# Kernel tuning notes

Hardware: AMD Instinct MI355X
Metric: run time of the kernel (lower is better)

## Reference

```python
import math
import jax, jax.numpy as jnp
import numpy as np

EPS = 1e-5
KS = 8          # emb_ks == emb_hs
NH = 4          # attention heads
LOOKBACK = 5
NLAYERS = 4


def prelu(x, a):
    return jnp.where(x >= 0, x, a * x)


def ln_c(x, g, b):
    # LayerNormalization4D: stats over channel dim; note (std + eps) denominator
    mu = jnp.mean(x, 1, keepdims=True)
    var = jnp.mean((x - mu) ** 2, 1, keepdims=True)
    return (x - mu) / (jnp.sqrt(var + EPS) + EPS) * g[None, :, None, None] + b[None, :, None, None]


def ln_cf_head(x, g, b):
    # x: [H, B, E, T, F]; stats over (E, F); g, b: [H, E, F]
    mu = jnp.mean(x, (2, 4), keepdims=True)
    var = jnp.mean((x - mu) ** 2, (2, 4), keepdims=True)
    return (x - mu) / (jnp.sqrt(var + EPS) + EPS) * g[:, None, :, None, :] + b[:, None, :, None, :]


def ln_cf_proj(x, g, b):
    # x: [B, C, T, F]; stats over (C, F); g, b: [C, F]
    mu = jnp.mean(x, (1, 3), keepdims=True)
    var = jnp.mean((x - mu) ** 2, (1, 3), keepdims=True)
    return (x - mu) / (jnp.sqrt(var + EPS) + EPS) * g[None, :, None, :] + b[None, :, None, :]


def lstm(x, wih, whh, bih, bhh):
    # x: [N, T, I] -> hidden sequence [N, T, H]; PyTorch gate order i, f, g, o
    xp = jnp.einsum('nti,gi->ntg', x, wih) + bih + bhh
    H = whh.shape[1]
    N = x.shape[0]

    def step(carry, xt):
        h, c = carry
        gates = xt + h @ whh.T
        i, f, g, o = jnp.split(gates, 4, axis=-1)
        c = jax.nn.sigmoid(f) * c + jax.nn.sigmoid(i) * jnp.tanh(g)
        h = jax.nn.sigmoid(o) * jnp.tanh(c)
        return (h, c), h

    init = (jnp.zeros((N, H), x.dtype), jnp.zeros((N, H), x.dtype))
    _, hs = jax.lax.scan(step, init, jnp.swapaxes(xp, 0, 1))
    return jnp.swapaxes(hs, 0, 1)


def bilstm(x, wih, whh, bih, bhh):
    fwd = lstm(x, wih[0], whh[0], bih[0], bhh[0])
    bwd = lstm(x[:, ::-1], wih[1], whh[1], bih[1], bhh[1])[:, ::-1]
    return jnp.concatenate([fwd, bwd], -1)


def unfold1d(x):
    # non-overlapping unfold (ks == stride == KS): [N, C, L] -> [N, L//KS, C*KS]
    N, C, Lx = x.shape
    return x.reshape(N, C, Lx // KS, KS).transpose(0, 2, 1, 3).reshape(N, Lx // KS, C * KS)


def fold1d(h, w, b):
    # ConvTranspose1d with stride == kernel == KS; h: [N, Lp, D], w: [D, C, KS]
    y = jnp.einsum('nld,dck->nlck', h, w)
    N, Lp, C, K = y.shape
    return y.transpose(0, 2, 1, 3).reshape(N, C, Lp * K) + b[None, :, None]


def conv2d(x, w, b):
    y = jax.lax.conv_general_dilated(x, w, (1, 1), ((1, 1), (1, 1)),
                                     dimension_numbers=('NCHW', 'OIHW', 'NCHW'))
    return y + b[None, :, None, None]


def block(x, p):
    B, C, oT, oF = x.shape
    T = math.ceil((oT - KS) / KS) * KS + KS
    F = math.ceil((oF - KS) / KS) * KS + KS
    x = jnp.pad(x, ((0, 0), (0, 0), (0, T - oT), (0, F - oF)))
    input_ = x
    # intra (frequency) bidirectional LSTM
    z = ln_c(input_, p['intra_norm_g'], p['intra_norm_b'])
    z = z.transpose(0, 2, 1, 3).reshape(B * T, C, F)
    z = unfold1d(z)                                    # [B*T, F//KS, C*KS]
    h = bilstm(z, p['intra_wih'], p['intra_whh'], p['intra_bih'], p['intra_bhh'])
    z = fold1d(h, p['intra_lin_w'], p['intra_lin_b'])  # [B*T, C, F]
    intra = z.reshape(B, T, C, F).transpose(0, 2, 1, 3) + input_
    # inter (time) causal LSTM
    z = ln_c(intra, p['inter_norm_g'], p['inter_norm_b'])
    z = z.transpose(0, 3, 1, 2).reshape(B * F, C, T)
    z = unfold1d(z)                                    # [B*F, T//KS, C*KS]
    h = lstm(z, p['inter_wih'], p['inter_whh'], p['inter_bih'], p['inter_bhh'])
    z = fold1d(h, p['inter_lin_w'], p['inter_lin_b'])  # [B*F, C, T]
    inter = z.reshape(B, F, C, T).transpose(0, 2, 3, 1) + intra
    inter = inter[..., :oT, :oF]

    # per-head 1x1-conv QKV (batched over heads) + local causal attention
    def qkv(w, b, a, g, beta):
        y = jnp.einsum('bctf,hec->hbetf', inter, w) + b[:, None, :, None, None]
        y = prelu(y, a[:, None, None, None, None])
        return ln_cf_head(y, g, beta)

    Q = qkv(p['q_w'], p['q_b'], p['q_a'], p['q_g'], p['q_beta'])
    K = qkv(p['k_w'], p['k_b'], p['k_a'], p['k_g'], p['k_beta'])
    V = qkv(p['v_w'], p['v_b'], p['v_a'], p['v_g'], p['v_beta'])
    E = Q.shape[2]
    CV = V.shape[2]
    Qf = Q.transpose(0, 1, 3, 2, 4).reshape(NH, B, oT, E * oF)
    Kf = K.transpose(0, 1, 3, 2, 4).reshape(NH, B, oT, E * oF)
    Vf = V.transpose(0, 1, 3, 2, 4).reshape(NH, B, oT, CV * oF)
    attn = jnp.einsum('hbtd,hbsd->hbts', Qf, Kf) / jnp.sqrt(jnp.asarray(E * oF, Qf.dtype))
    t = jnp.arange(oT)
    d = t[:, None] - t[None, :]
    mask = (d >= 0) & (d <= LOOKBACK)      # causal with 5-frame lookback
    attn = jnp.where(mask, attn, -1e30)
    A = jax.nn.softmax(attn, axis=-1)
    O = jnp.einsum('hbts,hbsd->hbtd', A, Vf).reshape(NH, B, oT, CV, oF)
    O = O.transpose(1, 0, 3, 2, 4).reshape(B, NH * CV, oT, oF)
    y = jnp.einsum('bctf,dc->bdtf', O, p['proj_w']) + p['proj_b'][None, :, None, None]
    y = prelu(y, p['proj_a'])
    y = ln_cf_proj(y, p['proj_g'], p['proj_beta'])
    return y + inter


def _forward(x, conv_w, conv_b, gn_g, gn_b,
             intra_norm_g, intra_norm_b, intra_wih, intra_whh, intra_bih, intra_bhh,
             intra_lin_w, intra_lin_b,
             inter_norm_g, inter_norm_b, inter_wih, inter_whh, inter_bih, inter_bhh,
             inter_lin_w, inter_lin_b,
             q_w, q_b, q_a, q_g, q_beta,
             k_w, k_b, k_a, k_g, k_beta,
             v_w, v_b, v_a, v_g, v_beta,
             proj_w, proj_b, proj_a, proj_g, proj_beta,
             deconv_w, deconv_b):
    esti = conv2d(x, conv_w, conv_b)
    # GroupNorm(1, emb_dim): per-sample stats over (C, T, F), per-channel affine
    mu = jnp.mean(esti, (1, 2, 3), keepdims=True)
    var = jnp.mean((esti - mu) ** 2, (1, 2, 3), keepdims=True)
    esti = (esti - mu) / jnp.sqrt(var + EPS) * gn_g[None, :, None, None] + gn_b[None, :, None, None]
    stacked = dict(
        intra_norm_g=intra_norm_g, intra_norm_b=intra_norm_b,
        intra_wih=intra_wih, intra_whh=intra_whh, intra_bih=intra_bih, intra_bhh=intra_bhh,
        intra_lin_w=intra_lin_w, intra_lin_b=intra_lin_b,
        inter_norm_g=inter_norm_g, inter_norm_b=inter_norm_b,
        inter_wih=inter_wih, inter_whh=inter_whh, inter_bih=inter_bih, inter_bhh=inter_bhh,
        inter_lin_w=inter_lin_w, inter_lin_b=inter_lin_b,
        q_w=q_w, q_b=q_b, q_a=q_a, q_g=q_g, q_beta=q_beta,
        k_w=k_w, k_b=k_b, k_a=k_a, k_g=k_g, k_beta=k_beta,
        v_w=v_w, v_b=v_b, v_a=v_a, v_g=v_g, v_beta=v_beta,
        proj_w=proj_w, proj_b=proj_b, proj_a=proj_a, proj_g=proj_g, proj_beta=proj_beta,
    )
    for l in range(NLAYERS):
        p = {k: v[l] for k, v in stacked.items()}
        esti = block(esti, p)
    # ConvTranspose2d(k=3, s=1, p=1) == conv with spatially flipped, io-swapped kernel, pad 1
    w2 = jnp.flip(deconv_w, (2, 3)).transpose(1, 0, 2, 3)
    return conv2d(esti, w2, deconv_b)


def setup_inputs() -> dict:
    key = jax.random.key(0)
    keys = iter(jax.random.split(key, 80))

    def rn(shape, s=0.05):
        return jax.random.normal(next(keys), shape, jnp.float32) * s

    L, C, H, E, CV, FA = 4, 32, 256, 4, 8, 161
    IN = C * KS
    return dict(
        x=jax.random.normal(next(keys), (8, 2, 504, 161), jnp.float32),
        conv_w=rn((C, 2, 3, 3)), conv_b=jnp.zeros((C,), jnp.float32),
        gn_g=jnp.ones((C,), jnp.float32), gn_b=jnp.zeros((C,), jnp.float32),
        intra_norm_g=jnp.ones((L, C), jnp.float32), intra_norm_b=jnp.zeros((L, C), jnp.float32),
        intra_wih=rn((L, 2, 4 * H, IN)), intra_whh=rn((L, 2, 4 * H, H)),
        intra_bih=jnp.zeros((L, 2, 4 * H), jnp.float32), intra_bhh=jnp.zeros((L, 2, 4 * H), jnp.float32),
        intra_lin_w=rn((L, 2 * H, C, KS)), intra_lin_b=jnp.zeros((L, C), jnp.float32),
        inter_norm_g=jnp.ones((L, C), jnp.float32), inter_norm_b=jnp.zeros((L, C), jnp.float32),
        inter_wih=rn((L, 4 * H, IN)), inter_whh=rn((L, 4 * H, H)),
        inter_bih=jnp.zeros((L, 4 * H), jnp.float32), inter_bhh=jnp.zeros((L, 4 * H), jnp.float32),
        inter_lin_w=rn((L, H, C, KS)), inter_lin_b=jnp.zeros((L, C), jnp.float32),
        q_w=rn((L, NH, E, C)), q_b=jnp.zeros((L, NH, E), jnp.float32),
        q_a=jnp.full((L, NH), 0.25, jnp.float32),
        q_g=jnp.ones((L, NH, E, FA), jnp.float32), q_beta=jnp.zeros((L, NH, E, FA), jnp.float32),
        k_w=rn((L, NH, E, C)), k_b=jnp.zeros((L, NH, E), jnp.float32),
        k_a=jnp.full((L, NH), 0.25, jnp.float32),
        k_g=jnp.ones((L, NH, E, FA), jnp.float32), k_beta=jnp.zeros((L, NH, E, FA), jnp.float32),
        v_w=rn((L, NH, CV, C)), v_b=jnp.zeros((L, NH, CV), jnp.float32),
        v_a=jnp.full((L, NH), 0.25, jnp.float32),
        v_g=jnp.ones((L, NH, CV, FA), jnp.float32), v_beta=jnp.zeros((L, NH, CV, FA), jnp.float32),
        proj_w=rn((L, C, C)), proj_b=jnp.zeros((L, C), jnp.float32),
        proj_a=jnp.full((L,), 0.25, jnp.float32),
        proj_g=jnp.ones((L, C, FA), jnp.float32), proj_beta=jnp.zeros((L, C, FA), jnp.float32),
        deconv_w=rn((C, 2, 3, 3)), deconv_b=jnp.zeros((2,), jnp.float32),
    )


def reference(x, conv_w, conv_b, gn_g, gn_b,
              intra_norm_g, intra_norm_b, intra_wih, intra_whh, intra_bih, intra_bhh,
              intra_lin_w, intra_lin_b,
              inter_norm_g, inter_norm_b, inter_wih, inter_whh, inter_bih, inter_bhh,
              inter_lin_w, inter_lin_b,
              q_w, q_b, q_a, q_g, q_beta,
              k_w, k_b, k_a, k_g, k_beta,
              v_w, v_b, v_a, v_g, v_beta,
              proj_w, proj_b, proj_a, proj_g, proj_beta,
              deconv_w, deconv_b):
    return _forward(x, conv_w, conv_b, gn_g, gn_b,
                    intra_norm_g, intra_norm_b, intra_wih, intra_whh, intra_bih, intra_bhh,
                    intra_lin_w, intra_lin_b,
                    inter_norm_g, inter_norm_b, inter_wih, inter_whh, inter_bih, inter_bhh,
                    inter_lin_w, inter_lin_b,
                    q_w, q_b, q_a, q_g, q_beta,
                    k_w, k_b, k_a, k_g, k_beta,
                    v_w, v_b, v_a, v_g, v_beta,
                    proj_w, proj_b, proj_a, proj_g, proj_beta,
                    deconv_w, deconv_b)
```

## Files before the change

kernel.cpp:

```cpp
#include <hip/hip_runtime.h>
#include <hip/hip_bf16.h>
#include <math.h>

#define BB   8
#define CH   32
#define TT   504
#define FFp  168
#define OF   161
#define KSZ  8
#define HID  256
#define NG   1024
#define NHh  4
#define EE   4
#define CVv  8
#define N1   4032
#define N2   1344
#define LFi  21
#define LTi  63
#define EPSf 1e-5f

#define AS1 __attribute__((address_space(1)))
#define AS3 __attribute__((address_space(3)))

typedef __hip_bfloat16 bf16;
typedef __attribute__((ext_vector_type(8))) short s16x8;
typedef __attribute__((ext_vector_type(4))) float f32x4;

__device__ __forceinline__ float b2f(bf16 v) { return __bfloat162float(v); }
__device__ __forceinline__ bf16 f2b(float v) { return __float2bfloat16(v); }
__device__ __forceinline__ float us2f(unsigned short u) {
  return __uint_as_float(((unsigned)u) << 16);
}
__device__ __forceinline__ unsigned short f2bu(float v) {
  unsigned u = __float_as_uint(v);
  unsigned r = u + 0x7fffu + ((u >> 16) & 1u);
  return (unsigned short)(r >> 16);
}

__device__ __forceinline__ float sigm(float x) { return 1.f / (1.f + __expf(-x)); }
__device__ __forceinline__ float tanh_f(float x) {
  x = fminf(15.f, fmaxf(-15.f, x));
  float e = __expf(2.f * x);
  return (e - 1.f) / (e + 1.f);
}

__device__ __forceinline__ void block_reduce2(float& s1, float& s2, float* red) {
#pragma unroll
  for (int off = 32; off > 0; off >>= 1) {
    s1 += __shfl_down(s1, off, 64);
    s2 += __shfl_down(s2, off, 64);
  }
  int lane = threadIdx.x & 63, wv = threadIdx.x >> 6;
  __syncthreads();
  if (lane == 0) { red[wv * 2] = s1; red[wv * 2 + 1] = s2; }
  __syncthreads();
  s1 = red[0] + red[2] + red[4] + red[6];
  s2 = red[1] + red[3] + red[5] + red[7];
}

__global__ __launch_bounds__(192) void conv_in_k(const float* __restrict__ x,
                                                 const float* __restrict__ w,
                                                 const float* __restrict__ bias,
                                                 bf16* __restrict__ out) {
  __shared__ float xs[2 * 3 * (OF + 3)];
  int bt = blockIdx.x;
  int b = bt / TT, t = bt % TT;
  int tid = threadIdx.x;
  for (int i = tid; i < 2 * 3 * (OF + 3); i += 192) {
    int ci = i / (3 * (OF + 3));
    int rem = i % (3 * (OF + 3));
    int rr = rem / (OF + 3);
    int f = rem % (OF + 3);
    int ts = t + rr - 1;
    float v = 0.f;
    if (ts >= 0 && ts < TT && f < OF) v = x[((size_t)(b * 2 + ci) * TT + ts) * OF + f];
    xs[i] = v;
  }
  __syncthreads();
  int f = tid;
  if (f < OF) {
    float xv[2][3][3];
#pragma unroll
    for (int ci = 0; ci < 2; ci++)
#pragma unroll
      for (int kh = 0; kh < 3; kh++)
#pragma unroll
        for (int kw = 0; kw < 3; kw++) {
          int ff = f + kw - 1;
          xv[ci][kh][kw] = (ff < 0) ? 0.f : xs[(ci * 3 + kh) * (OF + 3) + ff];
        }
    for (int co = 0; co < CH; co++) {
      float acc = bias[co];
#pragma unroll
      for (int ci = 0; ci < 2; ci++)
#pragma unroll
        for (int kh = 0; kh < 3; kh++)
#pragma unroll
          for (int kw = 0; kw < 3; kw++)
            acc += xv[ci][kh][kw] * w[((co * 2 + ci) * 3 + kh) * 3 + kw];
      out[((size_t)(b * CH + co) * TT + t) * OF + f] = f2b(acc);
    }
  }
}

__global__ __launch_bounds__(256) void gn_reduce_k(const bf16* __restrict__ xin,
                                                   float* __restrict__ stats) {
  const int M = CH * TT * OF;
  int b = blockIdx.x >> 6;
  int part = blockIdx.x & 63;
  const bf16* p = xin + (size_t)b * M;
  float s1 = 0.f, s2 = 0.f;
  for (int i = part * 256 + threadIdx.x; i < M; i += 64 * 256) {
    float v = b2f(p[i]);
    s1 += v; s2 += v * v;
  }
  __shared__ float red[8];
  block_reduce2(s1, s2, red);
  if (threadIdx.x == 0) {
    atomicAdd(&stats[b * 2], s1);
    atomicAdd(&stats[b * 2 + 1], s2);
  }
}

__global__ __launch_bounds__(256) void gn_apply_k(const bf16* __restrict__ xin,
                                                  const float* __restrict__ stats,
                                                  const float* __restrict__ g,
                                                  const float* __restrict__ bb,
                                                  bf16* __restrict__ act) {
  int gid = blockIdx.x * 256 + threadIdx.x;
  int f = gid % FFp;
  int t = (gid / FFp) % TT;
  int c = (gid / (FFp * TT)) % CH;
  int b = gid / (FFp * TT * CH);
  float v = 0.f;
  if (f < OF) {
    const float M = (float)(CH * TT * OF);
    float mu = stats[b * 2] / M;
    float var = stats[b * 2 + 1] / M - mu * mu;
    float xv = b2f(xin[((size_t)(b * CH + c) * TT + t) * OF + f]);
    v = (xv - mu) * rsqrtf(var + EPSf) * g[c] + bb[c];
  }
  act[gid] = f2b(v);
}

__global__ __launch_bounds__(256) void ln_unfold_k(const bf16* __restrict__ xin,
                                                   const float* __restrict__ g,
                                                   const float* __restrict__ bb,
                                                   bf16* __restrict__ out, int mode) {
  __shared__ float sm[CH * FFp];
  __shared__ float mu_s[FFp], rs_s[FFp];
  int bt = blockIdx.x;
  int b = bt / TT, t = bt % TT;
  const bf16* base = xin + ((size_t)b * CH * TT + t) * FFp;
  for (int idx = threadIdx.x; idx < CH * FFp; idx += 256) {
    int c = idx / FFp, f = idx % FFp;
    sm[idx] = b2f(base[(size_t)c * TT * FFp + f]);
  }
  __syncthreads();
  if (threadIdx.x < FFp) {
    int f = threadIdx.x;
    float s1 = 0.f, s2 = 0.f;
#pragma unroll
    for (int c = 0; c < CH; c++) { float v = sm[c * FFp + f]; s1 += v; s2 += v * v; }
    float mu = s1 / CH;
    float var = s2 / CH - mu * mu;
    mu_s[f] = mu;
    rs_s[f] = 1.f / (sqrtf(var + EPSf) + EPSf);
  }
  __syncthreads();
  for (int idx = threadIdx.x; idx < CH * FFp; idx += 256) {
    int c = idx / FFp, f = idx % FFp;
    float v = (sm[idx] - mu_s[f]) * rs_s[f] * g[c] + bb[c];
    size_t o;
    if (mode == 0) {
      o = ((size_t)(f >> 3) * N1 + bt) * 256 + c * 8 + (f & 7);
    } else {
      int n = b * FFp + f;
      o = ((size_t)(t >> 3) * N2 + n) * 256 + c * 8 + (t & 7);
    }
    out[o] = f2b(v);
  }
}

__global__ __launch_bounds__(256) void lstm_prep_k(const float* __restrict__ wih0,
                                                   const float* __restrict__ whh0,
                                                   bf16* __restrict__ blob0) {
  int dir = blockIdx.y;
  const float* wih = wih0 + (size_t)dir * 262144;
  const float* whh = whh0 + (size_t)dir * 262144;
  unsigned short* blob = (unsigned short*)(blob0 + (size_t)dir * 524288);
  int gid = blockIdx.x * 256 + threadIdx.x;
  int lane = gid & 63;
  int ks = (gid >> 6) & 15;
  int nt = gid >> 10;
  int n = nt * 16 + (lane & 15);
  int kb = ks * 32 + (lane >> 4) * 8;
  unsigned short o8[8];
#pragma unroll
  for (int j = 0; j < 8; j++) {
    int k = kb + j;
    float v = (k < 256) ? wih[n * 256 + k] : whh[n * 256 + (k - 256)];
    o8[j] = f2bu(v);
  }
  *(uint4*)(blob + (size_t)gid * 8) = *(uint4*)o8;
}

__global__ __launch_bounds__(512) void lstm_mfma_k(const bf16* __restrict__ xz,
                                                   const bf16* __restrict__ blob0,
                                                   const float* __restrict__ bih0,
                                                   const float* __restrict__ bhh0,
                                                   bf16* __restrict__ hout,
                                                   int N, int Ls, int hstride, int bidir) {
  __shared__ __attribute__((aligned(16))) short afr[16 * 64 * 8];
  extern __shared__ __attribute__((aligned(16))) short bstage[];
  int tid = threadIdx.x;
  int w = tid >> 6, lane = tid & 63;
  int l15 = lane & 15, lq = lane >> 4;
  int dir = blockIdx.y;
  const short* blob = (const short*)(blob0 + (size_t)dir * 524288);
  const float* bih = bih0 + dir * NG;
  const float* bhh = bhh0 + dir * NG;
  int hoff = dir * 256;
  int n0 = blockIdx.x * 16;
  unsigned short* houtu = (unsigned short*)hout;
  const short* xzs = (const short*)xz;
  short* bst_w = bstage + w * 4096;

  float bias[4][2];
#pragma unroll
  for (int q = 0; q < 4; q++)
#pragma unroll
    for (int j = 0; j < 2; j++) {
      int n = q * 256 + (2 * w + j) * 16 + l15;
      bias[q][j] = bih[n] + bhh[n];
    }
  for (int i = tid; i < 8 * 64 * 8; i += 512) afr[8 * 64 * 8 + i] = 0;
  float cst[8];
#pragma unroll
  for (int i = 0; i < 8; i++) cst[i] = 0.f;

#define BQ_ISSUE(C)                                                              \
  {                                                                              \
    int a_ = (C) >> 3, r_ = (C) & 7;                                             \
    int nt_ = (r_ >> 1) * 16 + 2 * w + (r_ & 1);                                 \
    const short* gb_ = blob + (size_t)nt_ * 8192 + a_ * 2048 + lane * 8;         \
    short* lb_ = bst_w + ((C) & 1) * 2048;                                       \
    _Pragma("unroll")                                                            \
    for (int k_ = 0; k_ < 4; k_++)                                               \
      __builtin_amdgcn_global_load_lds((const AS1 void*)(gb_ + k_ * 512),        \
                                       (AS3 void*)(lb_ + k_ * 512), 16, 0, 0);   \
  }

  for (int st = 0; st < Ls; st++) {
    int t = (bidir && dir) ? (Ls - 1 - st) : st;
    {
      const short* gx = xzs + ((size_t)t * N + n0 + (lane & 15)) * 256 + (w * 4 + (lane >> 4)) * 8;
      __builtin_amdgcn_global_load_lds((const AS1 void*)gx, (AS3 void*)(afr + w * 512), 16, 0, 0);
    }
    BQ_ISSUE(0);
    BQ_ISSUE(1);
    __syncthreads();

    f32x4 acc[4][2];
#pragma unroll
    for (int q = 0; q < 4; q++)
#pragma unroll
      for (int j = 0; j < 2; j++)
        acc[q][j] = (f32x4){bias[q][j], bias[q][j], bias[q][j], bias[q][j]};

    s16x8 af[4];
#pragma unroll
    for (int c = 0; c < 32; c++) {
      int a = c >> 3, r = c & 7;
      int q = r >> 1, j = r & 1;
      if (r == 0) {
#pragma unroll
        for (int k = 0; k < 4; k++)
          af[k] = *(const s16x8*)(&afr[((a * 4 + k) * 64 + lane) * 8]);
      }
      __builtin_amdgcn_s_waitcnt(0x0F74);
      const short* lb = bst_w + (c & 1) * 2048;
#pragma unroll
      for (int k = 0; k < 4; k++) {
        s16x8 bf = *(const s16x8*)(lb + k * 512 + lane * 8);
        acc[q][j] = __builtin_amdgcn_mfma_f32_16x16x32_bf16(af[k], bf, acc[q][j], 0, 0, 0);
      }
      if (c < 30) BQ_ISSUE(c + 2);
    }
    __syncthreads();

#pragma unroll
    for (int j = 0; j < 2; j++) {
      int d = (2 * w + j) * 16 + l15;
      int slot = (8 + (d >> 5)) * 64 + ((d >> 3) & 3) * 16;
#pragma unroll
      for (int r = 0; r < 4; r++) {
        int m = lq * 4 + r;
        float iv = sigm(acc[0][j][r]);
        float fv = sigm(acc[1][j][r]);
        float gv = tanh_f(acc[2][j][r]);
        float ov = sigm(acc[3][j][r]);
        float c = fv * cst[j * 4 + r] + iv * gv;
        cst[j * 4 + r] = c;
        float h = ov * tanh_f(c);
        unsigned short hb = f2bu(h);
        houtu[((size_t)t * N + n0 + m) * hstride + hoff + d] = hb;
        afr[(slot + m) * 8 + (d & 7)] = (short)hb;
      }
    }
  }
#undef BQ_ISSUE
}

__global__ __launch_bounds__(256) void fold_gemm_k(const bf16* __restrict__ A,
                                                   const float* __restrict__ Bw,
                                                   const float* __restrict__ linb,
                                                   const bf16* __restrict__ resid,
                                                   bf16* __restrict__ outp,
                                                   int K, int mode) {
  __shared__ float As[16 * 68];
  __shared__ float Bs[16 * 64];
  int tid = threadIdx.x;
  int n0 = blockIdx.x * 64;
  int m0 = blockIdx.y * 64;
  int tr = tid >> 4, tc = tid & 15;
  float acc[4][4] = {};
  int arow = tid >> 2, akg = (tid & 3) * 4;
  int bkk = tid >> 4, bc4 = (tid & 15) * 4;
  for (int k0 = 0; k0 < K; k0 += 16) {
    ushort4 avu = *(const ushort4*)((const unsigned short*)A + (size_t)(m0 + arow) * K + k0 + akg);
    float4 bv = *(const float4*)(Bw + (size_t)(k0 + bkk) * 256 + n0 + bc4);
    __syncthreads();
    As[(akg + 0) * 68 + arow] = us2f(avu.x);
    As[(akg + 1) * 68 + arow] = us2f(avu.y);
    As[(akg + 2) * 68 + arow] = us2f(avu.z);
    As[(akg + 3) * 68 + arow] = us2f(avu.w);
    *(float4*)(&Bs[bkk * 64 + bc4]) = bv;
    __syncthreads();
#pragma unroll
    for (int kk = 0; kk < 16; kk++) {
      float4 a4 = *(const float4*)(&As[kk * 68 + tr * 4]);
      float4 b4 = *(const float4*)(&Bs[kk * 64 + tc * 4]);
      float aa[4] = {a4.x, a4.y, a4.z, a4.w};
      float bb_[4] = {b4.x, b4.y, b4.z, b4.w};
#pragma unroll
      for (int i = 0; i < 4; i++)
#pragma unroll
        for (int j = 0; j < 4; j++) acc[i][j] += aa[i] * bb_[j];
    }
  }
#pragma unroll
  for (int i = 0; i < 4; i++) {
    int r = m0 + tr * 4 + i;
#pragma unroll
    for (int j = 0; j < 4; j++) {
      int col = n0 + tc * 4 + j;
      int c = col >> 3, kp = col & 7;
      float v = acc[i][j] + linb[c];
      if (mode == 0) {
        int l = r / N1, n = r % N1;
        int b = n / TT, t = n % TT;
        size_t o = ((size_t)(b * CH + c) * TT + t) * FFp + (l * 8 + kp);
        outp[o] = f2b(v + b2f(resid[o]));
      } else {
        int l = r / N2, n = r % N2;
        int b = n / FFp, fq = n % FFp;
        int t = l * 8 + kp;
        if (fq < OF) {
          size_t o = ((size_t)(b * CH + c) * TT + t) * OF + fq;
          size_t ri = ((size_t)(b * CH + c) * TT + t) * FFp + fq;
          outp[o] = f2b(v + b2f(resid[ri]));
        }
      }
    }
  }
}

__global__ __launch_bounds__(256) void qkv_k(const bf16* __restrict__ interc,
    const float* __restrict__ qw, const float* __restrict__ qb, const float* __restrict__ qa,
    const float* __restrict__ qg, const float* __restrict__ qbeta,
    const float* __restrict__ kw, const float* __restrict__ kb, const float* __restrict__ ka,
    const float* __restrict__ kg, const float* __restrict__ kbeta,
    const float* __restrict__ vw, const float* __restrict__ vb, const float* __restrict__ va,
    const float* __restrict__ vg, const float* __restrict__ vbeta,
    bf16* __restrict__ qo, bf16* __restrict__ ko, bf16* __restrict__ vo) {
  __shared__ float sm[CH * OF];
  __shared__ float wb[16 * 32];
  __shared__ float wbias[16];
  __shared__ float yb[16 * OF];
  __shared__ float red[8];
  int bt = blockIdx.x, h = blockIdx.y;
  int b = bt / TT, t = bt % TT;
  int tid = threadIdx.x;
  const bf16* src = interc + ((size_t)b * CH * TT + t) * OF;
  for (int idx = tid; idx < CH * OF; idx += 256) {
    int c = idx / OF, f = idx % OF;
    sm[idx] = b2f(src[(size_t)c * TT * OF + f]);
  }
  for (int idx = tid; idx < 512; idx += 256) {
    int e = idx >> 5, c = idx & 31;
    float w;
    if (e < 4) w = qw[(h * 4 + e) * 32 + c];
    else if (e < 8) w = kw[(h * 4 + e - 4) * 32 + c];
    else w = vw[(h * 8 + e - 8) * 32 + c];
    wb[idx] = w;
  }
  if (tid < 16) {
    float bv;
    if (tid < 4) bv = qb[h * 4 + tid];
    else if (tid < 8) bv = kb[h * 4 + tid - 4];
    else bv = vb[h * 8 + tid - 8];
    wbias[tid] = bv;
  }
  __syncthreads();
  float aQ = qa[h], aK = ka[h], aV = va[h];
  for (int idx = tid; idx < 16 * OF; idx += 256) {
    int e = idx / OF, f = idx % OF;
    float accv = wbias[e];
#pragma unroll
    for (int c = 0; c < 32; c++) accv += sm[c * OF + f] * wb[e * 32 + c];
    float a = e < 4 ? aQ : (e < 8 ? aK : aV);
    yb[idx] = accv >= 0.f ? accv : a * accv;
  }
  __syncthreads();
  for (int seg = 0; seg < 3; seg++) {
    int s0 = (seg == 0) ? 0 : ((seg == 1) ? 644 : 1288);
    int len = (seg == 2) ? 1288 : 644;
    float s1 = 0.f, s2 = 0.f;
    for (int i = tid; i < len; i += 256) { float v = yb[s0 + i]; s1 += v; s2 += v * v; }
    block_reduce2(s1, s2, red);
    float mu = s1 / len;
    float var = s2 / len - mu * mu;
    float rs = 1.f / (sqrtf(var + EPSf) + EPSf);
    const float* gp; const float* bp; bf16* op; int nch;
    if (seg == 0) { gp = qg; bp = qbeta; op = qo; nch = 4; }
    else if (seg == 1) { gp = kg; bp = kbeta; op = ko; nch = 4; }
    else { gp = vg; bp = vbeta; op = vo; nch = 8; }
    for (int i = tid; i < len; i += 256) {
      int e = i / OF, f = i % OF;
      float v = (yb[s0 + i] - mu) * rs * gp[(h * nch + e) * OF + f] + bp[(h * nch + e) * OF + f];
      op[(((size_t)(h * BB + b) * nch + e) * TT + t) * OF + f] = f2b(v);
    }
  }
}

__global__ __launch_bounds__(256) void attn_k(const bf16* __restrict__ Q,
                                              const bf16* __restrict__ Kt,
                                              const bf16* __restrict__ V,
                                              bf16* __restrict__ O) {
  int t = blockIdx.x;
  int hb = blockIdx.y;
  int h = hb >> 3, b = hb & 7;
  int tid = threadIdx.x;
  int nv = min(t, 5) + 1;
  const float scale = 0.0394055201f;
  __shared__ float redl[24];
  float part[6] = {0, 0, 0, 0, 0, 0};
  size_t qkbase = ((size_t)(h * BB + b) * EE) * TT * OF;
  for (int i = tid; i < EE * OF; i += 256) {
    int e = i / OF, f = i % OF;
    float qv = b2f(Q[qkbase + ((size_t)e * TT + t) * OF + f]);
#pragma unroll
    for (int d = 0; d < 6; d++)
      if (d < nv) part[d] += qv * b2f(Kt[qkbase + ((size_t)e * TT + (t - d)) * OF + f]);
  }
#pragma unroll
  for (int d = 0; d < 6; d++)
#pragma unroll
    for (int off = 32; off > 0; off >>= 1) part[d] += __shfl_down(part[d], off, 64);
  int lane = tid & 63, wv = tid >> 6;
  if (lane == 0) {
#pragma unroll
    for (int d = 0; d < 6; d++) redl[wv * 6 + d] = part[d];
  }
  __syncthreads();
  float a[6], sv[6];
  float m = -1e30f;
#pragma unroll
  for (int d = 0; d < 6; d++)
    if (d < nv) {
      float s = (redl[d] + redl[6 + d] + redl[12 + d] + redl[18 + d]) * scale;
      sv[d] = s;
      m = fmaxf(m, s);
    }
  float denom = 0.f;
#pragma unroll
  for (int d = 0; d < 6; d++)
    if (d < nv) { a[d] = __expf(sv[d] - m); denom += a[d]; }
  float inv = 1.f / denom;
  size_t vbase = ((size_t)(h * BB + b) * CVv) * TT * OF;
  for (int i = tid; i < CVv * OF; i += 256) {
    int cv = i / OF, f = i % OF;
    float o = 0.f;
#pragma unroll
    for (int d = 0; d < 6; d++)
      if (d < nv) o += a[d] * b2f(V[vbase + ((size_t)cv * TT + (t - d)) * OF + f]);
    O[(((size_t)b * CH + h * CVv + cv) * TT + t) * OF + f] = f2b(o * inv);
  }
}

__global__ __launch_bounds__(256) void proj_k(const bf16* __restrict__ ob,
                                              const float* __restrict__ pw,
                                              const float* __restrict__ pb,
                                              const float* __restrict__ pa,
                                              const float* __restrict__ pg,
                                              const float* __restrict__ pbeta,
                                              const bf16* __restrict__ interc,
                                              bf16* __restrict__ act) {
  __shared__ float sm[CH * OF];
  __shared__ float wsm[CH * CH];
  __shared__ float yb[CH * OF];
  __shared__ float red[8];
  int bt = blockIdx.x;
  int b = bt / TT, t = bt % TT;
  int tid = threadIdx.x;
  const bf16* src = ob + ((size_t)b * CH * TT + t) * OF;
  for (int idx = tid; idx < CH * OF; idx += 256) {
    int c = idx / OF, f = idx % OF;
    sm[idx] = b2f(src[(size_t)c * TT * OF + f]);
  }
  for (int idx = tid; idx < CH * CH; idx += 256) wsm[idx] = pw[idx];
  __syncthreads();
  float aP = pa[0];
  for (int idx = tid; idx < CH * OF; idx += 256) {
    int d = idx / OF, f = idx % OF;
    float accv = pb[d];
#pragma unroll
    for (int c = 0; c < 32; c++) accv += sm[c * OF + f] * wsm[d * 32 + c];
    yb[idx] = accv >= 0.f ? accv : aP * accv;
  }
  __syncthreads();
  float s1 = 0.f, s2 = 0.f;
  for (int i = tid; i < CH * OF; i += 256) { float v = yb[i]; s1 += v; s2 += v * v; }
  block_reduce2(s1, s2, red);
  const float Mn = (float)(CH * OF);
  float mu = s1 / Mn;
  float var = s2 / Mn - mu * mu;
  float rs = 1.f / (sqrtf(var + EPSf) + EPSf);
  for (int idx = tid; idx < CH * FFp; idx += 256) {
    int d = idx / FFp, f = idx % FFp;
    float v = 0.f;
    if (f < OF) {
      float y = (yb[d * OF + f] - mu) * rs * pg[d * OF + f] + pbeta[d * OF + f];
      v = y + b2f(interc[((size_t)(b * CH + d) * TT + t) * OF + f]);
    }
    act[((size_t)(b * CH + d) * TT + t) * FFp + f] = f2b(v);
  }
}

__global__ __launch_bounds__(256) void deconv_k(const bf16* __restrict__ act,
                                                const float* __restrict__ w,
                                                const float* __restrict__ bias,
                                                float* __restrict__ out) {
  __shared__ float ash[CH * 3 * FFp];
  int bt = blockIdx.x;
  int b = bt / TT, t = bt % TT;
  int tid = threadIdx.x;
  const short* acts = (const short*)act;
  for (int ch = tid; ch < CH * 3 * (FFp / 8); ch += 256) {
    int ci = ch / 63, rem = ch % 63;
    int rr = rem / 21, fc = rem % 21;
    int ts = t + rr - 1;
    float* dst = &ash[(ci * 3 + rr) * FFp + fc * 8];
    if (ts < 0 || ts >= TT) {
#pragma unroll
      for (int k2 = 0; k2 < 8; k2++) dst[k2] = 0.f;
    } else {
      s16x8 v = *(const s16x8*)(acts + ((size_t)(b * CH + ci) * TT + ts) * FFp + fc * 8);
#pragma unroll
      for (int k2 = 0; k2 < 8; k2++) dst[k2] = us2f((unsigned short)v[k2]);
    }
  }
  __syncthreads();
  int f = tid;
  if (f < OF) {
    float acc0 = bias[0], acc1 = bias[1];
#pragma unroll 4
    for (int ci = 0; ci < CH; ci++) {
      const float* row = &ash[ci * 3 * FFp];
      float xv[3][3];
#pragma unroll
      for (int kh = 0; kh < 3; kh++)
#pragma unroll
        for (int kw = 0; kw < 3; kw++) {
          int ff = f + kw - 1;
          xv[kh][kw] = (ff < 0) ? 0.f : row[kh * FFp + ff];
        }
#pragma unroll
      for (int kh = 0; kh < 3; kh++)
#pragma unroll
        for (int kw = 0; kw < 3; kw++) {
          acc0 += xv[kh][kw] * w[((ci * 2 + 0) * 3 + (2 - kh)) * 3 + (2 - kw)];
          acc1 += xv[kh][kw] * w[((ci * 2 + 1) * 3 + (2 - kh)) * 3 + (2 - kw)];
        }
    }
    out[((size_t)(b * 2 + 0) * TT + t) * OF + f] = acc0;
    out[((size_t)(b * 2 + 1) * TT + t) * OF + f] = acc1;
  }
}

extern "C" void kernel_launch(void* const* d_in, const int* in_sizes, int n_in,
                              void* d_out, int out_size, void* d_ws, size_t ws_size,
                              hipStream_t stream) {
  const float* x            = (const float*)d_in[0];
  const float* conv_w       = (const float*)d_in[1];
  const float* conv_b       = (const float*)d_in[2];
  const float* gn_g         = (const float*)d_in[3];
  const float* gn_b         = (const float*)d_in[4];
  const float* intra_norm_g = (const float*)d_in[5];
  const float* intra_norm_b = (const float*)d_in[6];
  const float* intra_wih    = (const float*)d_in[7];
  const float* intra_whh    = (const float*)d_in[8];
  const float* intra_bih    = (const float*)d_in[9];
  const float* intra_bhh    = (const float*)d_in[10];
  const float* intra_lin_w  = (const float*)d_in[11];
  const float* intra_lin_b  = (const float*)d_in[12];
  const float* inter_norm_g = (const float*)d_in[13];
  const float* inter_norm_b = (const float*)d_in[14];
  const float* inter_wih    = (const float*)d_in[15];
  const float* inter_whh    = (const float*)d_in[16];
  const float* inter_bih    = (const float*)d_in[17];
  const float* inter_bhh    = (const float*)d_in[18];
  const float* inter_lin_w  = (const float*)d_in[19];
  const float* inter_lin_b  = (const float*)d_in[20];
  const float* q_w    = (const float*)d_in[21];
  const float* q_b    = (const float*)d_in[22];
  const float* q_a    = (const float*)d_in[23];
  const float* q_g    = (const float*)d_in[24];
  const float* q_beta = (const float*)d_in[25];
  const float* k_w    = (const float*)d_in[26];
  const float* k_b    = (const float*)d_in[27];
  const float* k_a    = (const float*)d_in[28];
  const float* k_g    = (const float*)d_in[29];
  const float* k_beta = (const float*)d_in[30];
  const float* v_w    = (const float*)d_in[31];
  const float* v_b    = (const float*)d_in[32];
  const float* v_a    = (const float*)d_in[33];
  const float* v_g    = (const float*)d_in[34];
  const float* v_beta = (const float*)d_in[35];
  const float* proj_w    = (const float*)d_in[36];
  const float* proj_b    = (const float*)d_in[37];
  const float* proj_a    = (const float*)d_in[38];
  const float* proj_g    = (const float*)d_in[39];
  const float* proj_beta = (const float*)d_in[40];
  const float* deconv_w  = (const float*)d_in[41];
  const float* deconv_b  = (const float*)d_in[42];

  float* stats = (float*)d_ws;
  bf16* arena  = (bf16*)((char*)d_ws + 256);
  bf16* act    = arena;
  bf16* tmp    = arena + 21676032;
  bf16* hbuf   = arena + 43352064;
  bf16* res    = arena + 86704128;
  bf16* interc = arena + 108380160;
  bf16* convout = interc;
  bf16* qbuf = act;
  bf16* kbuf = tmp;
  bf16* vbuf = res;
  bf16* obuf = hbuf;
  bf16* blob_intra = res;
  bf16* blob_inter = interc;

  hipMemsetAsync(stats, 0, 64 * sizeof(float), stream);
  conv_in_k<<<4032, 192, 0, stream>>>(x, conv_w, conv_b, convout);
  gn_reduce_k<<<512, 256, 0, stream>>>(convout, stats);
  gn_apply_k<<<84672, 256, 0, stream>>>(convout, stats, gn_g, gn_b, act);

  for (int l = 0; l < 4; l++) {
    lstm_prep_k<<<dim3(256, 2), 256, 0, stream>>>(
        intra_wih + (size_t)l * 524288, intra_whh + (size_t)l * 524288, blob_intra);
    ln_unfold_k<<<4032, 256, 0, stream>>>(act, intra_norm_g + l * 32, intra_norm_b + l * 32, tmp, 0);
    lstm_mfma_k<<<dim3(252, 2), 512, 65536, stream>>>(
        tmp, blob_intra, intra_bih + l * 2048, intra_bhh + l * 2048, hbuf, N1, LFi, 512, 1);
    fold_gemm_k<<<dim3(4, 1323), 256, 0, stream>>>(
        hbuf, intra_lin_w + (size_t)l * 131072, intra_lin_b + l * 32, act, res, 512, 0);
    lstm_prep_k<<<dim3(256, 1), 256, 0, stream>>>(
        inter_wih + (size_t)l * 262144, inter_whh + (size_t)l * 262144, blob_inter);
    ln_unfold_k<<<4032, 256, 0, stream>>>(res, inter_norm_g + l * 32, inter_norm_b + l * 32, tmp, 1);
    lstm_mfma_k<<<dim3(84, 1), 512, 65536, stream>>>(
        tmp, blob_inter, inter_bih + l * 1024, inter_bhh + l * 1024, hbuf, N2, LTi, 256, 0);
    fold_gemm_k<<<dim3(4, 1323), 256, 0, stream>>>(
        hbuf, inter_lin_w + (size_t)l * 65536, inter_lin_b + l * 32, res, interc, 256, 1);
    qkv_k<<<dim3(4032, 4), 256, 0, stream>>>(interc,
        q_w + l * 512, q_b + l * 16, q_a + l * 4, q_g + l * 2576, q_beta + l * 2576,
        k_w + l * 512, k_b + l * 16, k_a + l * 4, k_g + l * 2576, k_beta + l * 2576,
        v_w + l * 1024, v_b + l * 32, v_a + l * 4, v_g + l * 5152, v_beta + l * 5152,
        qbuf, kbuf, vbuf);
    attn_k<<<dim3(504, 32), 256, 0, stream>>>(qbuf, kbuf, vbuf, obuf);
    proj_k<<<4032, 256, 0, stream>>>(obuf, proj_w + l * 1024, proj_b + l * 32, proj_a + l,
                                     proj_g + l * 5152, proj_beta + l * 5152, interc, act);
  }
  deconv_k<<<4032, 256, 0, stream>>>(act, deconv_w, deconv_b, (float*)d_out);
}
```

Before: 16.51 ms.

## Vectorize LN-unfold stores, add 8-timestep inter unfold, deepen LSTM weight prefetch

The LayerNorm+unfold kernel now writes eight packed bf16 values per 16-byte store instead of scattered 2-byte stores. The inter path gets a new kernel that processes 8 timesteps per block so the t-minor unfold output can be written as contiguous vectors. The LSTM MFMA loop splits each weight chunk in half and uses a 4-slot LDS ring with a 3-deep prefetch to better overlap global-to-LDS loads with MFMAs. The risks are higher LDS use in the new unfold kernel (about 100KB per block, which limits occupancy) and a waitcnt value that was not retuned for the new issue depth.

```diff
diff --git a/kernel.cpp b/kernel.cpp
--- a/kernel.cpp
+++ b/kernel.cpp
@@ -146,19 +146,22 @@
 __global__ __launch_bounds__(256) void ln_unfold_k(const bf16* __restrict__ xin,
                                                    const float* __restrict__ g,
                                                    const float* __restrict__ bb,
-                                                   bf16* __restrict__ out, int mode) {
+                                                   bf16* __restrict__ out) {
   __shared__ float sm[CH * FFp];
   __shared__ float mu_s[FFp], rs_s[FFp];
+  __shared__ float gg[CH], bv[CH];
   int bt = blockIdx.x;
   int b = bt / TT, t = bt % TT;
+  int tid = threadIdx.x;
+  if (tid < CH) { gg[tid] = g[tid]; bv[tid] = bb[tid]; }
   const bf16* base = xin + ((size_t)b * CH * TT + t) * FFp;
-  for (int idx = threadIdx.x; idx < CH * FFp; idx += 256) {
+  for (int idx = tid; idx < CH * FFp; idx += 256) {
     int c = idx / FFp, f = idx % FFp;
     sm[idx] = b2f(base[(size_t)c * TT * FFp + f]);
   }
   __syncthreads();
-  if (threadIdx.x < FFp) {
-    int f = threadIdx.x;
+  if (tid < FFp) {
+    int f = tid;
     float s1 = 0.f, s2 = 0.f;
 #pragma unroll
     for (int c = 0; c < CH; c++) { float v = sm[c * FFp + f]; s1 += v; s2 += v * v; }
@@ -168,17 +171,66 @@
     rs_s[f] = 1.f / (sqrtf(var + EPSf) + EPSf);
   }
   __syncthreads();
-  for (int idx = threadIdx.x; idx < CH * FFp; idx += 256) {
-    int c = idx / FFp, f = idx % FFp;
-    float v = (sm[idx] - mu_s[f]) * rs_s[f] * g[c] + bb[c];
-    size_t o;
-    if (mode == 0) {
-      o = ((size_t)(f >> 3) * N1 + bt) * 256 + c * 8 + (f & 7);
-    } else {
-      int n = b * FFp + f;
-      o = ((size_t)(t >> 3) * N2 + n) * 256 + c * 8 + (t & 7);
-    }
-    out[o] = f2b(v);
+  unsigned short* outu = (unsigned short*)out;
+  for (int ch = tid; ch < LFi * CH; ch += 256) {
+    int gI = ch >> 5, c = ch & 31;
+    float gc = gg[c], bc = bv[c];
+    unsigned short o8[8];
+#pragma unroll
+    for (int k = 0; k < 8; k++) {
+      int f = gI * 8 + k;
+      float v = (sm[c * FFp + f] - mu_s[f]) * rs_s[f] * gc + bc;
+      o8[k] = f2bu(v);
+    }
+    *(uint4*)(outu + ((size_t)gI * N1 + bt) * 256 + c * 8) = *(uint4*)o8;
+  }
+}
+
+__global__ __launch_bounds__(256) void ln_unfold8_k(const bf16* __restrict__ xin,
+                                                    const float* __restrict__ g,
+                                                    const float* __restrict__ bb,
+                                                    bf16* __restrict__ out) {
+  __shared__ short smb[8 * CH * FFp];
+  __shared__ float mu_s[8 * FFp], rs_s[8 * FFp];
+  __shared__ float gg[CH], bv[CH];
+  int tg = blockIdx.x, b = blockIdx.y;
+  int tid = threadIdx.x;
+  if (tid < CH) { gg[tid] = g[tid]; bv[tid] = bb[tid]; }
+  const short* src = (const short*)xin;
+  for (int idx = tid; idx < 8 * CH * (FFp / 8); idx += 256) {
+    int t8 = idx / (CH * 21);
+    int rem = idx % (CH * 21);
+    int c = rem / 21, fc = rem % 21;
+    s16x8 v = *(const s16x8*)(src + ((size_t)(b * CH + c) * TT + tg * 8 + t8) * FFp + fc * 8);
+    *(s16x8*)(&smb[(t8 * CH + c) * FFp + fc * 8]) = v;
+  }
+  __syncthreads();
+  for (int p = tid; p < 8 * FFp; p += 256) {
+    int t8 = p / FFp, f = p % FFp;
+    float s1 = 0.f, s2 = 0.f;
+#pragma unroll
+    for (int c = 0; c < CH; c++) {
+      float v = us2f((unsigned short)smb[(t8 * CH + c) * FFp + f]);
+      s1 += v; s2 += v * v;
+    }
+    float mu = s1 / CH;
+    float var = s2 / CH - mu * mu;
+    mu_s[p] = mu;
+    rs_s[p] = 1.f / (sqrtf(var + EPSf) + EPSf);
+  }
+  __syncthreads();
+  unsigned short* outu = (unsigned short*)out;
+  for (int ch = tid; ch < FFp * CH; ch += 256) {
+    int f = ch >> 5, c = ch & 31;
+    float gc = gg[c], bc = bv[c];
+    unsigned short o8[8];
+#pragma unroll
+    for (int k = 0; k < 8; k++) {
+      float v = us2f((unsigned short)smb[(k * CH + c) * FFp + f]);
+      v = (v - mu_s[k * FFp + f]) * rs_s[k * FFp + f] * gc + bc;
+      o8[k] = f2bu(v);
+    }
+    *(uint4*)(outu + ((size_t)tg * N2 + b * FFp + f) * 256 + c * 8) = *(uint4*)o8;
   }
 }
 
@@ -241,12 +293,13 @@
 
 #define BQ_ISSUE(C)                                                              \
   {                                                                              \
-    int a_ = (C) >> 3, r_ = (C) & 7;                                             \
+    int c32_ = (C) >> 1, h2_ = (C) & 1;                                          \
+    int a_ = c32_ >> 3, r_ = c32_ & 7;                                           \
     int nt_ = (r_ >> 1) * 16 + 2 * w + (r_ & 1);                                 \
-    const short* gb_ = blob + (size_t)nt_ * 8192 + a_ * 2048 + lane * 8;         \
-    short* lb_ = bst_w + ((C) & 1) * 2048;                                       \
+    const short* gb_ = blob + (size_t)nt_ * 8192 + (a_ * 4 + h2_ * 2) * 512 + lane * 8; \
+    short* lb_ = bst_w + ((C) & 3) * 1024;                                       \
     _Pragma("unroll")                                                            \
-    for (int k_ = 0; k_ < 4; k_++)                                               \
+    for (int k_ = 0; k_ < 2; k_++)                                               \
       __builtin_amdgcn_global_load_lds((const AS1 void*)(gb_ + k_ * 512),        \
                                        (AS3 void*)(lb_ + k_ * 512), 16, 0, 0);   \
   }
@@ -259,6 +312,7 @@
     }
     BQ_ISSUE(0);
     BQ_ISSUE(1);
+    BQ_ISSUE(2);
     __syncthreads();
 
     f32x4 acc[4][2];
@@ -270,22 +324,23 @@
 
     s16x8 af[4];
 #pragma unroll
-    for (int c = 0; c < 32; c++) {
-      int a = c >> 3, r = c & 7;
+    for (int C = 0; C < 64; C++) {
+      int c32 = C >> 1, h2 = C & 1;
+      int a = c32 >> 3, r = c32 & 7;
       int q = r >> 1, j = r & 1;
-      if (r == 0) {
+      if (r == 0 && h2 == 0) {
 #pragma unroll
         for (int k = 0; k < 4; k++)
           af[k] = *(const s16x8*)(&afr[((a * 4 + k) * 64 + lane) * 8]);
       }
       __builtin_amdgcn_s_waitcnt(0x0F74);
-      const short* lb = bst_w + (c & 1) * 2048;
-#pragma unroll
-      for (int k = 0; k < 4; k++) {
+      const short* lb = bst_w + (C & 3) * 1024;
+#pragma unroll
+      for (int k = 0; k < 2; k++) {
         s16x8 bf = *(const s16x8*)(lb + k * 512 + lane * 8);
-        acc[q][j] = __builtin_amdgcn_mfma_f32_16x16x32_bf16(af[k], bf, acc[q][j], 0, 0, 0);
+        acc[q][j] = __builtin_amdgcn_mfma_f32_16x16x32_bf16(af[h2 * 2 + k], bf, acc[q][j], 0, 0, 0);
       }
-      if (c < 30) BQ_ISSUE(c + 2);
+      if (C < 61) BQ_ISSUE(C + 3);
     }
     __syncthreads();
 
@@ -669,14 +724,14 @@
   for (int l = 0; l < 4; l++) {
     lstm_prep_k<<<dim3(256, 2), 256, 0, stream>>>(
         intra_wih + (size_t)l * 524288, intra_whh + (size_t)l * 524288, blob_intra);
-    ln_unfold_k<<<4032, 256, 0, stream>>>(act, intra_norm_g + l * 32, intra_norm_b + l * 32, tmp, 0);
+    ln_unfold_k<<<4032, 256, 0, stream>>>(act, intra_norm_g + l * 32, intra_norm_b + l * 32, tmp);
     lstm_mfma_k<<<dim3(252, 2), 512, 65536, stream>>>(
         tmp, blob_intra, intra_bih + l * 2048, intra_bhh + l * 2048, hbuf, N1, LFi, 512, 1);
     fold_gemm_k<<<dim3(4, 1323), 256, 0, stream>>>(
         hbuf, intra_lin_w + (size_t)l * 131072, intra_lin_b + l * 32, act, res, 512, 0);
     lstm_prep_k<<<dim3(256, 1), 256, 0, stream>>>(
         inter_wih + (size_t)l * 262144, inter_whh + (size_t)l * 262144, blob_inter);
-    ln_unfold_k<<<4032, 256, 0, stream>>>(res, inter_norm_g + l * 32, inter_norm_b + l * 32, tmp, 1);
+    ln_unfold8_k<<<dim3(LTi, BB), 256, 0, stream>>>(res, inter_norm_g + l * 32, inter_norm_b + l * 32, tmp);
     lstm_mfma_k<<<dim3(84, 1), 512, 65536, stream>>>(
         tmp, blob_inter, inter_bih + l * 1024, inter_bhh + l * 1024, hbuf, N2, LTi, 256, 0);
     fold_gemm_k<<<dim3(4, 1323), 256, 0, stream>>>(
```

After: 16.47 ms. No clear change (-0.2%).
